# Performance work log

Hardware: AMD Instinct MI355X
Metric: run time of the kernel (lower is better)

The kernel has to match this reference:

```python
import jax, jax.numpy as jnp
import numpy as np

NUM_HEADS = 16
HEAD_DIM = 64
MEMORY_SIZE = 65536
K_SIMILAR = 8
K_CONTIGUOUS = 2
SURPRISE_THRESHOLD = 0.5
EPS = 1e-8  # torch F.cosine_similarity eps


def setup_inputs() -> dict:
    key = jax.random.key(0)
    ks = jax.random.split(key, 6)
    B, H, S, HD = 4, NUM_HEADS, 8192, HEAD_DIM
    D = H * HD
    inputs = jax.random.normal(ks[0], (B, S, D), dtype=jnp.float32)
    q = jax.random.normal(ks[1], (B, H, S, HD), dtype=jnp.float32)
    k = jax.random.normal(ks[2], (B, H, S, HD), dtype=jnp.float32)
    v = jax.random.normal(ks[3], (B, H, S, HD), dtype=jnp.float32)
    attention_mask = jnp.ones((B, S), dtype=jnp.float32)
    events = jax.random.normal(ks[4], (MEMORY_SIZE, D), dtype=jnp.float32)
    return {"inputs": inputs, "q": q, "k": k, "v": v,
            "attention_mask": attention_mask, "events": events,
            "seq_len_q": 8192}


def _segment_mean(kf, seg, S):
    # kf: [S, D], seg: [S] int32 segment ids (exclusive cumsum of boundary mask)
    sums = jax.ops.segment_sum(kf, seg, num_segments=S)          # [S, D]
    cnts = jax.ops.segment_sum(jnp.ones_like(seg, jnp.float32), seg, num_segments=S)
    means = sums / jnp.maximum(cnts, 1.0)[:, None]
    return means, cnts


def reference(inputs, q, k, v, attention_mask, events, seq_len_q):
    B, H, S, HD = k.shape
    D = H * HD
    # flatten keys per token: [B, S, H*HD]
    kf = k.transpose(0, 2, 1, 3).reshape(B, S, D)

    # --- surprise scores: ||k_t - k_{t-1}|| padded with 0 at t=0 ---
    diffs = kf[:, 1:] - kf[:, :-1]
    norms = jnp.linalg.norm(diffs, axis=-1)                      # [B, S-1]
    surprise = jnp.pad(norms, ((0, 0), (1, 0)))                  # [B, S]

    # --- event segmentation (threshold = mean + c*std, unbiased std like torch) ---
    mean = jnp.mean(surprise, axis=1, keepdims=True)
    std = jnp.std(surprise, axis=1, ddof=1, keepdims=True)
    bmask = surprise > (mean + SURPRISE_THRESHOLD * std)
    bmask = bmask.at[:, -1].set(True)                            # last index is always a boundary
    bi = bmask.astype(jnp.int32)
    seg = jnp.cumsum(bi, axis=1) - bi                            # token t -> #boundaries before t

    # --- memory update: mean-pool keys within each event (scatter) ---
    new_events, event_lengths = jax.vmap(_segment_mean, in_axes=(0, 0, None))(kf, seg, S)
    # new_events: [B, S, D] (rows >= num_events are zero), event_lengths: [B, S]

    # --- retrieval: cosine sim of last-token key vs memory, top-k gather ---
    query = kf[:, -1]                                            # [B, D]
    qn = jnp.maximum(jnp.linalg.norm(query, axis=-1), EPS)       # [B]
    en = jnp.maximum(jnp.linalg.norm(events, axis=-1), EPS)      # [M]
    sims = (query @ events.T) / (qn[:, None] * en[None, :])      # [B, M]
    kt = min(K_SIMILAR + K_CONTIGUOUS, events.shape[0])
    _, idx = jax.lax.top_k(sims, kt)                             # [B, kt]

    ret = events[idx]                                            # [B, kt, D]
    ret = ret.reshape(B, kt, H, HD).transpose(0, 2, 1, 3)        # [B, H, kt, HD]
    ret_k, ret_v = ret, ret                                      # non-differential: v == k slice

    aug_k = jnp.concatenate([ret_k, k], axis=2)                  # [B, H, kt+S, HD]
    aug_v = jnp.concatenate([ret_v, v], axis=2)
    aug_mask = jnp.concatenate([jnp.ones((B, kt), attention_mask.dtype), attention_mask], axis=1)

    cp = seq_len_q - 1
    ret_pos = jnp.linspace(float(cp - kt), float(cp - 1), kt, dtype=jnp.float32)
    pos = jnp.arange(S, dtype=jnp.float32)
    aug_positions = jnp.broadcast_to(jnp.concatenate([ret_pos, pos]), (B, kt + S))

    return (inputs, q, aug_k, aug_v, aug_mask, aug_positions, new_events, event_lengths)
```

## Files before the change

### kernel.cpp

```cpp
#include <hip/hip_runtime.h>
#include <math.h>

#define BB 4
#define HH 16
#define SS 8192
#define HDD 64
#define DD 1024
#define MEM 65536
#define KT 10

static const long O0 = 0;
static const long O1 = 33554432;
static const long O2 = 67108864;
static const long O3 = 100704256;
static const long O4 = 134299648;
static const long O5 = 134332456;
static const long O6 = 134365264;
static const long O7 = 167919696;

#define WS_NEED_FUSED 5767168UL

#define N4REG 8388608L

typedef float __attribute__((ext_vector_type(4))) f4v;

static __device__ __forceinline__ void nt_store4(float4* p, float4 v) {
    f4v t; t.x = v.x; t.y = v.y; t.z = v.z; t.w = v.w;
    __builtin_nontemporal_store(t, (f4v*)p);
}
static __device__ __forceinline__ float4 nt_load4(const float4* p) {
    f4v t = __builtin_nontemporal_load((const f4v*)p);
    float4 v; v.x = t.x; v.y = t.y; v.z = t.z; v.w = t.w;
    return v;
}

#define R0_BLOCKS 4096
#define R1_BLOCKS 16384
#define R2_BLOCKS 2048
__global__ __launch_bounds__(256) void bigfused_kernel(
        const float4* __restrict__ in0, const float4* __restrict__ q,
        const float4* __restrict__ k4, const float* __restrict__ kf,
        const float4* __restrict__ v, const float4* __restrict__ events4,
        float4* __restrict__ out4, double* __restrict__ partial,
        float* __restrict__ sims, int do_part) {
    __shared__ float4 qls4[BB][256];
    int blk = blockIdx.x;
    int tid = threadIdx.x;
    if (blk < R0_BLOCKS) {
        int band = blk >> 10;
        long i = ((long)(blk & 1023)) * 256 + tid;
        const long bstride = 1024L * 256;
        if (band == 0) {
            for (; i < N4REG; i += bstride)
                nt_store4(out4 + (O0 >> 2) + i, nt_load4(in0 + i));
        } else if (band == 1) {
            for (; i < N4REG; i += bstride)
                nt_store4(out4 + (O1 >> 2) + i, nt_load4(q + i));
        } else if (band == 3) {
            for (; i < N4REG; i += bstride) {
                long chunk = i >> 17;
                long r = i & 131071;
                nt_store4(out4 + (O3 >> 2) + chunk * 131232 + 160 + r,
                          nt_load4(v + i));
            }
        } else {
            for (; i < N4REG; i += bstride) {
                long chunk = i >> 17;
                long r = i & 131071;
                float4 cur = k4[i];
                nt_store4(out4 + (O2 >> 2) + chunk * 131232 + 160 + r, cur);
                if (do_part) {
                    int s = (int)(r >> 4);
                    if (s > 0) {
                        float4 pv = k4[i - 16];
                        double dx = (double)cur.x - (double)pv.x;
                        double dy = (double)cur.y - (double)pv.y;
                        double dz = (double)cur.z - (double)pv.z;
                        double dw = (double)cur.w - (double)pv.w;
                        double acc = dx * dx + dy * dy + dz * dz + dw * dw;
                        acc += __shfl_xor(acc, 1, 64);
                        acc += __shfl_xor(acc, 2, 64);
                        acc += __shfl_xor(acc, 4, 64);
                        acc += __shfl_xor(acc, 8, 64);
                        if ((tid & 15) == 0) {
                            int b = (int)(chunk >> 4);
                            int h = (int)(chunk & 15);
                            partial[((long)b * SS + s) * HH + h] = acc;
                        }
                    }
                }
            }
        }
    } else if (blk < R0_BLOCKS + R1_BLOCKS) {
        for (int j = tid; j < BB * 256; j += 256) {
            int b = j >> 8;
            int f4i = j & 255;
            qls4[b][f4i] =
                k4[((long)(b * HH + (f4i >> 4)) * SS + (SS - 1)) * 16 + (f4i & 15)];
        }
        __syncthreads();
        int w = tid >> 6;
        int lane = tid & 63;
        long e = (long)(blk - R0_BLOCKS) * 4 + w;
        const float4* er = events4 + e * 256;
        float en = 0.f, d0 = 0.f, d1 = 0.f, d2 = 0.f, d3 = 0.f;
#pragma unroll
        for (int it = 0; it < 4; ++it) {
            int j4 = lane + it * 64;
            float4 ev = nt_load4(er + j4);
            en += ev.x * ev.x + ev.y * ev.y + ev.z * ev.z + ev.w * ev.w;
            float4 q0 = qls4[0][j4];
            d0 += ev.x * q0.x + ev.y * q0.y + ev.z * q0.z + ev.w * q0.w;
            float4 q1 = qls4[1][j4];
            d1 += ev.x * q1.x + ev.y * q1.y + ev.z * q1.z + ev.w * q1.w;
            float4 q2 = qls4[2][j4];
            d2 += ev.x * q2.x + ev.y * q2.y + ev.z * q2.z + ev.w * q2.w;
            float4 q3 = qls4[3][j4];
            d3 += ev.x * q3.x + ev.y * q3.y + ev.z * q3.z + ev.w * q3.w;
        }
        for (int m = 32; m >= 1; m >>= 1) {
            en += __shfl_xor(en, m, 64);
            d0 += __shfl_xor(d0, m, 64);
            d1 += __shfl_xor(d1, m, 64);
            d2 += __shfl_xor(d2, m, 64);
            d3 += __shfl_xor(d3, m, 64);
        }
        if (lane == 0) {
            float enn = fmaxf(sqrtf(en), 1e-8f);
            sims[0 * (long)MEM + e] = d0 / enn;
            sims[1 * (long)MEM + e] = d1 / enn;
            sims[2 * (long)MEM + e] = d2 / enn;
            sims[3 * (long)MEM + e] = d3 / enn;
        }
    } else {
        long i = ((long)(blk - R0_BLOCKS - R1_BLOCKS)) * 256 + tid;
        const long stride = (long)R2_BLOCKS * 256;
        const float4 z = make_float4(0.f, 0.f, 0.f, 0.f);
        for (; i < 8396800L; i += stride) {
            if (i < 8388608L)
                nt_store4(out4 + (O6 >> 2) + i, z);
            else
                nt_store4(out4 + (O7 >> 2) + (i - 8388608L), z);
        }
    }
}

__global__ __launch_bounds__(256) void surprise_fallback_kernel(
        const float* __restrict__ k, double* __restrict__ surprise) {
    int wid = (int)(((long)blockIdx.x * blockDim.x + threadIdx.x) >> 6);
    int lane = threadIdx.x & 63;
    if (wid >= BB * SS) return;
    int b = wid >> 13;
    int s = wid & (SS - 1);
    double acc = 0.0;
    if (s > 0) {
        const float* kb = k + (long)b * HH * SS * HDD;
        for (int h = 0; h < HH; ++h) {
            long off = ((long)h * SS + s) * HDD + lane;
            double d = (double)kb[off] - (double)kb[off - HDD];
            acc += d * d;
        }
        for (int m = 32; m >= 1; m >>= 1) acc += __shfl_xor(acc, m, 64);
    }
    if (lane == 0) surprise[wid] = (s == 0) ? 0.0 : sqrt(acc);
}

__global__ __launch_bounds__(1024) void stats_scan_kernel(
        const double* __restrict__ partial, const double* __restrict__ surprise,
        int* __restrict__ bpos, int* __restrict__ nseg, int fused) {
    int b = blockIdx.x;
    int tid = threadIdx.x;
    double loc[8];
    double sum = 0.0;
    if (fused) {
        const double* pb = partial + (long)b * SS * HH;
        for (int j = 0; j < 8; ++j) {
            int s = tid * 8 + j;
            double acc = 0.0;
            if (s > 0) {
                const double* row = pb + (long)s * HH;
                for (int h = 0; h < HH; ++h) acc += row[h];
            }
            loc[j] = (s == 0) ? 0.0 : sqrt(acc);
            sum += loc[j];
        }
    } else {
        const double* sp = surprise + (long)b * SS;
        for (int j = 0; j < 8; ++j) { loc[j] = sp[tid * 8 + j]; sum += loc[j]; }
    }
    __shared__ double sd[1024];
    sd[tid] = sum;
    __syncthreads();
    for (int off = 512; off >= 1; off >>= 1) {
        if (tid < off) sd[tid] += sd[tid + off];
        __syncthreads();
    }
    double mean = sd[0] / SS;
    __syncthreads();
    double vs = 0.0;
    for (int j = 0; j < 8; ++j) { double d = loc[j] - mean; vs += d * d; }
    sd[tid] = vs;
    __syncthreads();
    for (int off = 512; off >= 1; off >>= 1) {
        if (tid < off) sd[tid] += sd[tid + off];
        __syncthreads();
    }
    double thr = mean + 0.5 * sqrt(sd[0] / (SS - 1));
    __syncthreads();

    int bi[8];
    int cnt = 0;
    for (int j = 0; j < 8; ++j) {
        int s = tid * 8 + j;
        bi[j] = (s == SS - 1) || (loc[j] > thr);
        cnt += bi[j];
    }
    __shared__ int si[1024];
    si[tid] = cnt;
    __syncthreads();
    for (int off = 1; off < 1024; off <<= 1) {
        int v = 0;
        if (tid >= off) v = si[tid - off];
        __syncthreads();
        si[tid] += v;
        __syncthreads();
    }
    int run = si[tid] - cnt;
    for (int j = 0; j < 8; ++j) {
        if (bi[j]) { bpos[(long)b * SS + run] = tid * 8 + j; ++run; }
    }
    if (tid == 1023) nseg[b] = si[1023];
}

__global__ __launch_bounds__(256) void topk_part_kernel(
        const float* __restrict__ sims, float* __restrict__ cval,
        int* __restrict__ cidx) {
    int blk = blockIdx.x;
    int b = blk >> 4;
    int part = blk & 15;
    const float* sb = sims + (long)b * MEM + part * 4096;
    int base = part * 4096;
    int tid = threadIdx.x;
    __shared__ float bv[256];
    __shared__ int bix[256];
    __shared__ int chosen[KT];
    for (int p = 0; p < KT; ++p) {
        float best = -INFINITY;
        int bi = 0x7fffffff;
        for (int it = 0; it < 16; ++it) {
            int e = tid + it * 256;
            bool skip = false;
            for (int c = 0; c < p; ++c)
                if (chosen[c] == e) skip = true;
            if (skip) continue;
            float v = sb[e];
            if (v > best) { best = v; bi = e; }
        }
        bv[tid] = best;
        bix[tid] = bi;
        __syncthreads();
        for (int off = 128; off >= 1; off >>= 1) {
            if (tid < off) {
                if (bv[tid + off] > bv[tid] ||
                    (bv[tid + off] == bv[tid] && bix[tid + off] < bix[tid])) {
                    bv[tid] = bv[tid + off];
                    bix[tid] = bix[tid + off];
                }
            }
            __syncthreads();
        }
        if (tid == 0) {
            chosen[p] = bix[0];
            cval[blk * KT + p] = bv[0];
            cidx[blk * KT + p] = base + bix[0];
        }
        __syncthreads();
    }
}

__global__ __launch_bounds__(256) void topk_merge_kernel(
        const float* __restrict__ cval, const int* __restrict__ cidx,
        int* __restrict__ idxout) {
    int b = blockIdx.x;
    int tid = threadIdx.x;
    __shared__ float v[256];
    __shared__ int ix[256];
    float mv = -INFINITY;
    int mi = 0x7fffffff;
    if (tid < 160) { mv = cval[b * 160 + tid]; mi = cidx[b * 160 + tid]; }
    v[tid] = mv;
    ix[tid] = mi;
    __syncthreads();
    if (tid == 0) {
        for (int p = 0; p < KT; ++p) {
            float best = -INFINITY;
            int bi = 0x7fffffff;
            int bslot = 0;
            for (int j = 0; j < 160; ++j) {
                if (v[j] > best || (v[j] == best && ix[j] < bi)) {
                    best = v[j];
                    bi = ix[j];
                    bslot = j;
                }
            }
            idxout[b * KT + p] = bi;
            v[bslot] = -INFINITY;
            ix[bslot] = 0x7fffffff;
        }
    }
}

__global__ __launch_bounds__(256) void tail_kernel(
        const float* __restrict__ events, const int* __restrict__ idxin,
        const float* __restrict__ amask, const void* __restrict__ seqp,
        float* __restrict__ out) {
    int blk = blockIdx.x;
    int tid = threadIdx.x;
    if (blk < BB * KT) {
        int b = blk / KT;
        int t = blk % KT;
        int ev = idxin[b * KT + t];
        for (int c = 0; c < 4; ++c) {
            int j = tid + c * 256;
            float vv = events[(long)ev * DD + j];
            int h = j >> 6;
            int d = j & 63;
            long dst = (((long)b * HH + h) * (SS + KT) + t) * HDD + d;
            out[O2 + dst] = vv;
            out[O3 + dst] = vv;
        }
    } else {
        int iv = ((const int*)seqp)[0];
        int seqlen;
        if (iv > 0 && iv < (1 << 24)) seqlen = iv;
        else seqlen = (int)(((const float*)seqp)[0]);
        int cp = seqlen - 1;
        int n = BB * (SS + KT);
        int i = (blk - BB * KT) * 256 + tid;
        int stride = 64 * 256;
        for (; i < n; i += stride) {
            int b = i / (SS + KT);
            int t = i - b * (SS + KT);
            out[O4 + i] = (t < KT) ? 1.0f : amask[(long)b * SS + t - KT];
            out[O5 + i] = (t < KT) ? (float)(cp - KT + t) : (float)(t - KT);
        }
    }
}

__global__ __launch_bounds__(256) void segmean_kernel(
        const float4* __restrict__ k4, const int* __restrict__ bpos,
        const int* __restrict__ nseg, float4* __restrict__ ne4,
        float* __restrict__ event_lengths) {
    int j = blockIdx.x;
    int b = blockIdx.y;
    int ns = nseg[b];
    if (j >= ns) return;
    int tid = threadIdx.x;
    float4* row = ne4 + ((long)b * SS + j) * 256;
    int start = (j == 0) ? 0 : bpos[(long)b * SS + j - 1] + 1;
    int end = bpos[(long)b * SS + j];
    const float4* kb = k4 + ((long)(b * HH + (tid >> 4)) * SS) * 16 + (tid & 15);
    double a0 = 0.0, a1 = 0.0, a2 = 0.0, a3 = 0.0;
    for (int s = start; s <= end; ++s) {
        float4 x = kb[(long)s * 16];
        a0 += (double)x.x;
        a1 += (double)x.y;
        a2 += (double)x.z;
        a3 += (double)x.w;
    }
    double inv = 1.0 / (double)(end - start + 1);
    nt_store4(row + tid, make_float4((float)(a0 * inv), (float)(a1 * inv),
                                     (float)(a2 * inv), (float)(a3 * inv)));
    if (tid == 0) event_lengths[(long)b * SS + j] = (float)(end - start + 1);
}

extern "C" void kernel_launch(void* const* d_in, const int* in_sizes, int n_in,
                              void* d_out, int out_size, void* d_ws, size_t ws_size,
                              hipStream_t stream) {
    const float* in_inputs = (const float*)d_in[0];
    const float* in_q = (const float*)d_in[1];
    const float* in_k = (const float*)d_in[2];
    const float* in_v = (const float*)d_in[3];
    const float* in_amask = (const float*)d_in[4];
    const float* in_events = (const float*)d_in[5];
    const void* in_seq = d_in[6];
    float* out = (float*)d_out;

    char* ws = (char*)d_ws;
    double* surprise = (double*)ws;
    float* sims = (float*)(ws + 262144);
    int* bpos = (int*)(ws + 1310720);
    int* nseg = (int*)(ws + 1441792);
    int* idxw = (int*)(ws + 1441824);
    float* cval = (float*)(ws + 1442304);
    int* cidx = (int*)(ws + 1444864);
    double* partial = (double*)(ws + 1572864);

    const int fused = (ws_size >= WS_NEED_FUSED) ? 1 : 0;

    bigfused_kernel<<<R0_BLOCKS + R1_BLOCKS + R2_BLOCKS, 256, 0, stream>>>(
        (const float4*)in_inputs, (const float4*)in_q, (const float4*)in_k,
        in_k, (const float4*)in_v, (const float4*)in_events, (float4*)out,
        partial, sims, fused);
    if (!fused)
        surprise_fallback_kernel<<<8192, 256, 0, stream>>>(in_k, surprise);
    stats_scan_kernel<<<4, 1024, 0, stream>>>(partial, surprise, bpos, nseg,
                                              fused);
    topk_part_kernel<<<BB * 16, 256, 0, stream>>>(sims, cval, cidx);
    topk_merge_kernel<<<BB, 256, 0, stream>>>(cval, cidx, idxw);
    tail_kernel<<<BB * KT + 64, 256, 0, stream>>>(in_events, idxw, in_amask,
                                                  in_seq, out);
    dim3 sg(SS, BB);
    segmean_kernel<<<sg, 256, 0, stream>>>((const float4*)in_k, bpos, nseg,
                                           (float4*)(out + O6), out + O7);
}
```

Baseline: 501.9 us.

## Fuse segment mean with tail, parallelize surprise reduce, register top-k merge

Removes the upfront zero-fill of new_events; the segment-mean kernel now writes zeros for unused segment rows itself, and it is fused with the tail kernel. The segment mean reads keys back from the augmented output copy, which uses normal stores so it may stay in cache. The surprise partial reduction moves from a 4-block serial scan into its own 32-block kernel. Each sims block now handles 4 events in a loop. Top-k partition uses per-thread register lists plus a tree merge instead of 10 rounds of block reductions.

After: 433.5 us. 1.16x faster.

```diff
diff --git a/kernel.cpp b/kernel.cpp
--- a/kernel.cpp
+++ b/kernel.cpp
@@ -8,6 +8,7 @@
 #define DD 1024
 #define MEM 65536
 #define KT 10
+#define AUGROWS (SS + KT)
 
 static const long O0 = 0;
 static const long O1 = 33554432;
@@ -34,19 +35,17 @@
     return v;
 }
 
-#define R0_BLOCKS 4096
-#define R1_BLOCKS 16384
-#define R2_BLOCKS 2048
+#define COPY_BLOCKS 4096
+#define SIMS_BLOCKS 4096
 __global__ __launch_bounds__(256) void bigfused_kernel(
         const float4* __restrict__ in0, const float4* __restrict__ q,
-        const float4* __restrict__ k4, const float* __restrict__ kf,
-        const float4* __restrict__ v, const float4* __restrict__ events4,
-        float4* __restrict__ out4, double* __restrict__ partial,
-        float* __restrict__ sims, int do_part) {
+        const float4* __restrict__ k4, const float4* __restrict__ v,
+        const float4* __restrict__ events4, float4* __restrict__ out4,
+        double* __restrict__ partial, float* __restrict__ sims, int do_part) {
     __shared__ float4 qls4[BB][256];
     int blk = blockIdx.x;
     int tid = threadIdx.x;
-    if (blk < R0_BLOCKS) {
+    if (blk < COPY_BLOCKS) {
         int band = blk >> 10;
         long i = ((long)(blk & 1023)) * 256 + tid;
         const long bstride = 1024L * 256;
@@ -60,7 +59,7 @@
             for (; i < N4REG; i += bstride) {
                 long chunk = i >> 17;
                 long r = i & 131071;
-                nt_store4(out4 + (O3 >> 2) + chunk * 131232 + 160 + r,
+                nt_store4(out4 + (O3 >> 2) + chunk * 131232L + 160 + r,
                           nt_load4(v + i));
             }
         } else {
@@ -68,7 +67,7 @@
                 long chunk = i >> 17;
                 long r = i & 131071;
                 float4 cur = k4[i];
-                nt_store4(out4 + (O2 >> 2) + chunk * 131232 + 160 + r, cur);
+                out4[(O2 >> 2) + chunk * 131232L + 160 + r] = cur;
                 if (do_part) {
                     int s = (int)(r >> 4);
                     if (s > 0) {
@@ -91,7 +90,7 @@
                 }
             }
         }
-    } else if (blk < R0_BLOCKS + R1_BLOCKS) {
+    } else {
         for (int j = tid; j < BB * 256; j += 256) {
             int b = j >> 8;
             int f4i = j & 255;
@@ -101,48 +100,55 @@
         __syncthreads();
         int w = tid >> 6;
         int lane = tid & 63;
-        long e = (long)(blk - R0_BLOCKS) * 4 + w;
-        const float4* er = events4 + e * 256;
-        float en = 0.f, d0 = 0.f, d1 = 0.f, d2 = 0.f, d3 = 0.f;
-#pragma unroll
-        for (int it = 0; it < 4; ++it) {
-            int j4 = lane + it * 64;
-            float4 ev = nt_load4(er + j4);
-            en += ev.x * ev.x + ev.y * ev.y + ev.z * ev.z + ev.w * ev.w;
-            float4 q0 = qls4[0][j4];
-            d0 += ev.x * q0.x + ev.y * q0.y + ev.z * q0.z + ev.w * q0.w;
-            float4 q1 = qls4[1][j4];
-            d1 += ev.x * q1.x + ev.y * q1.y + ev.z * q1.z + ev.w * q1.w;
-            float4 q2 = qls4[2][j4];
-            d2 += ev.x * q2.x + ev.y * q2.y + ev.z * q2.z + ev.w * q2.w;
-            float4 q3 = qls4[3][j4];
-            d3 += ev.x * q3.x + ev.y * q3.y + ev.z * q3.z + ev.w * q3.w;
-        }
-        for (int m = 32; m >= 1; m >>= 1) {
-            en += __shfl_xor(en, m, 64);
-            d0 += __shfl_xor(d0, m, 64);
-            d1 += __shfl_xor(d1, m, 64);
-            d2 += __shfl_xor(d2, m, 64);
-            d3 += __shfl_xor(d3, m, 64);
-        }
-        if (lane == 0) {
-            float enn = fmaxf(sqrtf(en), 1e-8f);
-            sims[0 * (long)MEM + e] = d0 / enn;
-            sims[1 * (long)MEM + e] = d1 / enn;
-            sims[2 * (long)MEM + e] = d2 / enn;
-            sims[3 * (long)MEM + e] = d3 / enn;
-        }
-    } else {
-        long i = ((long)(blk - R0_BLOCKS - R1_BLOCKS)) * 256 + tid;
-        const long stride = (long)R2_BLOCKS * 256;
-        const float4 z = make_float4(0.f, 0.f, 0.f, 0.f);
-        for (; i < 8396800L; i += stride) {
-            if (i < 8388608L)
-                nt_store4(out4 + (O6 >> 2) + i, z);
-            else
-                nt_store4(out4 + (O7 >> 2) + (i - 8388608L), z);
-        }
-    }
+        long e0 = (long)(blk - COPY_BLOCKS) * 4 + w;
+        for (int rr = 0; rr < 4; ++rr) {
+            long e = e0 + (long)rr * (4 * SIMS_BLOCKS);
+            const float4* er = events4 + e * 256;
+            float en = 0.f, d0 = 0.f, d1 = 0.f, d2 = 0.f, d3 = 0.f;
+#pragma unroll
+            for (int it = 0; it < 4; ++it) {
+                int j4 = lane + it * 64;
+                float4 ev = nt_load4(er + j4);
+                en += ev.x * ev.x + ev.y * ev.y + ev.z * ev.z + ev.w * ev.w;
+                float4 q0 = qls4[0][j4];
+                d0 += ev.x * q0.x + ev.y * q0.y + ev.z * q0.z + ev.w * q0.w;
+                float4 q1 = qls4[1][j4];
+                d1 += ev.x * q1.x + ev.y * q1.y + ev.z * q1.z + ev.w * q1.w;
+                float4 q2 = qls4[2][j4];
+                d2 += ev.x * q2.x + ev.y * q2.y + ev.z * q2.z + ev.w * q2.w;
+                float4 q3 = qls4[3][j4];
+                d3 += ev.x * q3.x + ev.y * q3.y + ev.z * q3.z + ev.w * q3.w;
+            }
+            for (int m = 32; m >= 1; m >>= 1) {
+                en += __shfl_xor(en, m, 64);
+                d0 += __shfl_xor(d0, m, 64);
+                d1 += __shfl_xor(d1, m, 64);
+                d2 += __shfl_xor(d2, m, 64);
+                d3 += __shfl_xor(d3, m, 64);
+            }
+            if (lane == 0) {
+                float enn = fmaxf(sqrtf(en), 1e-8f);
+                sims[0 * (long)MEM + e] = d0 / enn;
+                sims[1 * (long)MEM + e] = d1 / enn;
+                sims[2 * (long)MEM + e] = d2 / enn;
+                sims[3 * (long)MEM + e] = d3 / enn;
+            }
+        }
+    }
+}
+
+__global__ __launch_bounds__(1024) void surprise_reduce_kernel(
+        const double* __restrict__ partial, double* __restrict__ surprise) {
+    int t = blockIdx.x * 1024 + threadIdx.x;
+    if (t >= BB * SS) return;
+    int s = t & (SS - 1);
+    double acc = 0.0;
+    if (s > 0) {
+        const double* row = partial + (long)t * HH;
+#pragma unroll
+        for (int h = 0; h < HH; ++h) acc += row[h];
+    }
+    surprise[t] = (s == 0) ? 0.0 : sqrt(acc);
 }
 
 __global__ __launch_bounds__(256) void surprise_fallback_kernel(
@@ -166,28 +172,14 @@
 }
 
 __global__ __launch_bounds__(1024) void stats_scan_kernel(
-        const double* __restrict__ partial, const double* __restrict__ surprise,
-        int* __restrict__ bpos, int* __restrict__ nseg, int fused) {
+        const double* __restrict__ surprise, int* __restrict__ bpos,
+        int* __restrict__ nseg) {
     int b = blockIdx.x;
     int tid = threadIdx.x;
+    const double* sp = surprise + (long)b * SS;
     double loc[8];
     double sum = 0.0;
-    if (fused) {
-        const double* pb = partial + (long)b * SS * HH;
-        for (int j = 0; j < 8; ++j) {
-            int s = tid * 8 + j;
-            double acc = 0.0;
-            if (s > 0) {
-                const double* row = pb + (long)s * HH;
-                for (int h = 0; h < HH; ++h) acc += row[h];
-            }
-            loc[j] = (s == 0) ? 0.0 : sqrt(acc);
-            sum += loc[j];
-        }
-    } else {
-        const double* sp = surprise + (long)b * SS;
-        for (int j = 0; j < 8; ++j) { loc[j] = sp[tid * 8 + j]; sum += loc[j]; }
-    }
+    for (int j = 0; j < 8; ++j) { loc[j] = sp[tid * 8 + j]; sum += loc[j]; }
     __shared__ double sd[1024];
     sd[tid] = sum;
     __syncthreads();
@@ -241,40 +233,64 @@
     const float* sb = sims + (long)b * MEM + part * 4096;
     int base = part * 4096;
     int tid = threadIdx.x;
-    __shared__ float bv[256];
-    __shared__ int bix[256];
-    __shared__ int chosen[KT];
-    for (int p = 0; p < KT; ++p) {
-        float best = -INFINITY;
-        int bi = 0x7fffffff;
-        for (int it = 0; it < 16; ++it) {
-            int e = tid + it * 256;
-            bool skip = false;
-            for (int c = 0; c < p; ++c)
-                if (chosen[c] == e) skip = true;
-            if (skip) continue;
-            float v = sb[e];
-            if (v > best) { best = v; bi = e; }
-        }
-        bv[tid] = best;
-        bix[tid] = bi;
-        __syncthreads();
-        for (int off = 128; off >= 1; off >>= 1) {
-            if (tid < off) {
-                if (bv[tid + off] > bv[tid] ||
-                    (bv[tid + off] == bv[tid] && bix[tid + off] < bix[tid])) {
-                    bv[tid] = bv[tid + off];
-                    bix[tid] = bix[tid + off];
+
+    float val[KT];
+    int idx[KT];
+#pragma unroll
+    for (int p = 0; p < KT; ++p) { val[p] = -INFINITY; idx[p] = 0x7fffffff; }
+    for (int it = 0; it < 16; ++it) {
+        int e = tid + it * 256;
+        float v = sb[e];
+        if (v > val[KT - 1]) {
+#pragma unroll
+            for (int p = KT - 1; p >= 1; --p) {
+                if (v > val[p - 1]) {
+                    val[p] = val[p - 1];
+                    idx[p] = idx[p - 1];
+                } else {
+                    val[p] = v;
+                    idx[p] = e;
+                    v = -INFINITY;
                 }
             }
-            __syncthreads();
-        }
-        if (tid == 0) {
-            chosen[p] = bix[0];
-            cval[blk * KT + p] = bv[0];
-            cidx[blk * KT + p] = base + bix[0];
-        }
-        __syncthreads();
+            if (v != -INFINITY) { val[0] = v; idx[0] = e; }
+        }
+    }
+    __shared__ float lv[256][KT];
+    __shared__ int li[256][KT];
+#pragma unroll
+    for (int p = 0; p < KT; ++p) { lv[tid][p] = val[p]; li[tid][p] = idx[p]; }
+    for (int off = 128; off >= 1; off >>= 1) {
+        __syncthreads();
+        if (tid < off) {
+            float a_[KT], b_[KT], m_[KT];
+            int ai_[KT], bi_[KT], mi_[KT];
+#pragma unroll
+            for (int p = 0; p < KT; ++p) {
+                a_[p] = lv[tid][p];
+                ai_[p] = li[tid][p];
+                b_[p] = lv[tid + off][p];
+                bi_[p] = li[tid + off][p];
+            }
+            int pa = 0, pb = 0;
+#pragma unroll
+            for (int p = 0; p < KT; ++p) {
+                bool ta = (a_[pa] > b_[pb]) ||
+                          (a_[pa] == b_[pb] && ai_[pa] < bi_[pb]);
+                if (ta) { m_[p] = a_[pa]; mi_[p] = ai_[pa]; ++pa; }
+                else    { m_[p] = b_[pb]; mi_[p] = bi_[pb]; ++pb; }
+            }
+#pragma unroll
+            for (int p = 0; p < KT; ++p) { lv[tid][p] = m_[p]; li[tid][p] = mi_[p]; }
+        }
+    }
+    __syncthreads();
+    if (tid == 0) {
+#pragma unroll
+        for (int p = 0; p < KT; ++p) {
+            cval[blk * KT + p] = lv[0][p];
+            cidx[blk * KT + p] = base + li[0][p];
+        }
     }
 }
 
@@ -310,22 +326,52 @@
     }
 }
 
-__global__ __launch_bounds__(256) void tail_kernel(
-        const float* __restrict__ events, const int* __restrict__ idxin,
-        const float* __restrict__ amask, const void* __restrict__ seqp,
-        float* __restrict__ out) {
+__global__ __launch_bounds__(256) void segtail_kernel(
+        const float4* __restrict__ out4c, const int* __restrict__ bpos,
+        const int* __restrict__ nseg, const float* __restrict__ events,
+        const int* __restrict__ idxin, const float* __restrict__ amask,
+        const void* __restrict__ seqp, float* __restrict__ out) {
     int blk = blockIdx.x;
     int tid = threadIdx.x;
-    if (blk < BB * KT) {
-        int b = blk / KT;
-        int t = blk % KT;
+    float4* ne4 = (float4*)(out + O6);
+    if (blk < BB * SS) {
+        int b = blk >> 13;
+        int j = blk & (SS - 1);
+        int ns = nseg[b];
+        float4* row = ne4 + ((long)b * SS + j) * 256;
+        if (j >= ns) {
+            nt_store4(row + tid, make_float4(0.f, 0.f, 0.f, 0.f));
+            if (tid == 0) out[O7 + (long)b * SS + j] = 0.0f;
+            return;
+        }
+        int start = (j == 0) ? 0 : bpos[(long)b * SS + j - 1] + 1;
+        int end = bpos[(long)b * SS + j];
+        const float4* kb = out4c + (O2 >> 2) +
+                           ((long)(b * HH + (tid >> 4)) * AUGROWS + KT) * 16 +
+                           (tid & 15);
+        double a0 = 0.0, a1 = 0.0, a2 = 0.0, a3 = 0.0;
+        for (int s = start; s <= end; ++s) {
+            float4 x = kb[(long)s * 16];
+            a0 += (double)x.x;
+            a1 += (double)x.y;
+            a2 += (double)x.z;
+            a3 += (double)x.w;
+        }
+        double inv = 1.0 / (double)(end - start + 1);
+        nt_store4(row + tid, make_float4((float)(a0 * inv), (float)(a1 * inv),
+                                         (float)(a2 * inv), (float)(a3 * inv)));
+        if (tid == 0) out[O7 + (long)b * SS + j] = (float)(end - start + 1);
+    } else if (blk < BB * SS + BB * KT) {
+        int g = blk - BB * SS;
+        int b = g / KT;
+        int t = g % KT;
         int ev = idxin[b * KT + t];
         for (int c = 0; c < 4; ++c) {
             int j = tid + c * 256;
             float vv = events[(long)ev * DD + j];
             int h = j >> 6;
             int d = j & 63;
-            long dst = (((long)b * HH + h) * (SS + KT) + t) * HDD + d;
+            long dst = (((long)b * HH + h) * AUGROWS + t) * HDD + d;
             out[O2 + dst] = vv;
             out[O3 + dst] = vv;
         }
@@ -335,43 +381,16 @@
         if (iv > 0 && iv < (1 << 24)) seqlen = iv;
         else seqlen = (int)(((const float*)seqp)[0]);
         int cp = seqlen - 1;
-        int n = BB * (SS + KT);
-        int i = (blk - BB * KT) * 256 + tid;
+        int n = BB * AUGROWS;
+        int i = (blk - BB * SS - BB * KT) * 256 + tid;
         int stride = 64 * 256;
         for (; i < n; i += stride) {
-            int b = i / (SS + KT);
-            int t = i - b * (SS + KT);
+            int b = i / AUGROWS;
+            int t = i - b * AUGROWS;
             out[O4 + i] = (t < KT) ? 1.0f : amask[(long)b * SS + t - KT];
             out[O5 + i] = (t < KT) ? (float)(cp - KT + t) : (float)(t - KT);
         }
     }
-}
-
-__global__ __launch_bounds__(256) void segmean_kernel(
-        const float4* __restrict__ k4, const int* __restrict__ bpos,
-        const int* __restrict__ nseg, float4* __restrict__ ne4,
-        float* __restrict__ event_lengths) {
-    int j = blockIdx.x;
-    int b = blockIdx.y;
-    int ns = nseg[b];
-    if (j >= ns) return;
-    int tid = threadIdx.x;
-    float4* row = ne4 + ((long)b * SS + j) * 256;
-    int start = (j == 0) ? 0 : bpos[(long)b * SS + j - 1] + 1;
-    int end = bpos[(long)b * SS + j];
-    const float4* kb = k4 + ((long)(b * HH + (tid >> 4)) * SS) * 16 + (tid & 15);
-    double a0 = 0.0, a1 = 0.0, a2 = 0.0, a3 = 0.0;
-    for (int s = start; s <= end; ++s) {
-        float4 x = kb[(long)s * 16];
-        a0 += (double)x.x;
-        a1 += (double)x.y;
-        a2 += (double)x.z;
-        a3 += (double)x.w;
-    }
-    double inv = 1.0 / (double)(end - start + 1);
-    nt_store4(row + tid, make_float4((float)(a0 * inv), (float)(a1 * inv),
-                                     (float)(a2 * inv), (float)(a3 * inv)));
-    if (tid == 0) event_lengths[(long)b * SS + j] = (float)(end - start + 1);
 }
 
 extern "C" void kernel_launch(void* const* d_in, const int* in_sizes, int n_in,
@@ -398,19 +417,18 @@
 
     const int fused = (ws_size >= WS_NEED_FUSED) ? 1 : 0;
 
-    bigfused_kernel<<<R0_BLOCKS + R1_BLOCKS + R2_BLOCKS, 256, 0, stream>>>(
+    bigfused_kernel<<<COPY_BLOCKS + SIMS_BLOCKS, 256, 0, stream>>>(
         (const float4*)in_inputs, (const float4*)in_q, (const float4*)in_k,
-        in_k, (const float4*)in_v, (const float4*)in_events, (float4*)out,
-        partial, sims, fused);
-    if (!fused)
+        (const float4*)in_v, (const float4*)in_events, (float4*)out, partial,
+        sims, fused);
+    if (fused) {
+        surprise_reduce_kernel<<<32, 1024, 0, stream>>>(partial, surprise);
+    } else {
         surprise_fallback_kernel<<<8192, 256, 0, stream>>>(in_k, surprise);
-    stats_scan_kernel<<<4, 1024, 0, stream>>>(partial, surprise, bpos, nseg,
-                                              fused);
+    }
+    stats_scan_kernel<<<4, 1024, 0, stream>>>(surprise, bpos, nseg);
     topk_part_kernel<<<BB * 16, 256, 0, stream>>>(sims, cval, cidx);
     topk_merge_kernel<<<BB, 256, 0, stream>>>(cval, cidx, idxw);
-    tail_kernel<<<BB * KT + 64, 256, 0, stream>>>(in_events, idxw, in_amask,
-                                                  in_seq, out);
-    dim3 sg(SS, BB);
-    segmean_kernel<<<sg, 256, 0, stream>>>((const float4*)in_k, bpos, nseg,
-                                           (float4*)(out + O6), out + O7);
-}
+    segtail_kernel<<<BB * SS + BB * KT + 64, 256, 0, stream>>>(
+        (const float4*)out, bpos, nseg, in_events, idxw, in_amask, in_seq, out);
+}
```
